# Kernel optimization log

Measured on AMD Instinct MI355X. Metric: run time of the kernel, lower is better.

Reference implementation:

```python
import jax, jax.numpy as jnp
import numpy as np

LENGTH, D, CHI, CLASSES = 784, 2, 128, 10
BATCH = 1024


def setup_inputs() -> dict:
    key = jax.random.key(0)
    k1, k2, k3 = jax.random.split(key, 3)
    # feature-mapped samples (batch, d, length), values in [0,1] like cossin map
    x = jax.random.uniform(k1, (BATCH, D, LENGTH), dtype=jnp.float32)
    # per-site residual weights; small init so the residual recurrence stays stable
    W = jax.random.normal(k2, (LENGTH, D, CHI, CHI), dtype=jnp.float32) * (0.01 / np.sqrt(CHI))
    # classifier matrix applied to the final hidden vector
    V = jax.random.normal(k3, (CHI, CLASSES), dtype=jnp.float32) / np.sqrt(CHI)
    return {"x": x, "W": W, "V": V}


def reference(x, W, V):
    # x: (B, d, L), W: (L, d, chi, chi), V: (chi, classes)
    B = x.shape[0]
    chi = W.shape[2]
    h0 = jnp.ones((B, chi), dtype=x.dtype)  # initial hidden bond vector

    xs = jnp.moveaxis(x, 2, 0)  # (L, B, d) so scan iterates over sites

    def site_step(h, inputs):
        xn, Wn = inputs  # xn: (B, d), Wn: (d, chi, chi)
        # residual MPS update: h <- h + sum_{s,a} x[n,s] W_n[s,a,b] h[a]
        h = h + jnp.einsum('ns,sab,na->nb', xn, Wn, h)
        return h, None

    h, _ = jax.lax.scan(site_step, h0, (xs, W))
    logits = h @ V  # (B, classes)
    return logits
```

## Files before the change

### kernel.cpp

```cpp
#include <hip/hip_runtime.h>

#define LL 784
#define CHI 128
#define CLS 10
#define BC 16
#define NBLK 64

typedef __attribute__((ext_vector_type(8))) short short8;
typedef __attribute__((ext_vector_type(4))) float floatx4;

__device__ inline unsigned int f2bf(float v) {
    unsigned int u = __float_as_uint(v);
    u += 0x7fffu + ((u >> 16) & 1u);
    return u >> 16;
}

__device__ inline void lds_barrier() {
    asm volatile("s_waitcnt lgkmcnt(0)\n\ts_barrier" ::: "memory");
}

__device__ inline float dpp_xor1(float v) {
    int r = __builtin_amdgcn_update_dpp(0, __float_as_int(v), 0xB1, 0xF, 0xF, true);
    return __int_as_float(r);
}

__global__ __launch_bounds__(256) void prep_kernel(const float* __restrict__ W,
                                                   uint4* __restrict__ ws4) {
    __shared__ float tile[32 * 132];
    const int b = blockIdx.x;
    const int n = b >> 3, s = (b >> 2) & 1, kt = b & 3;
    const float* Wp = W + ((size_t)(n * 2 + s) * CHI + kt * 32) * CHI;
    const int t = threadIdx.x;
    #pragma unroll
    for (int k = 0; k < 4; k++) {
        int v = t + k * 256;
        int a = v >> 5, c4 = v & 31;
        float4 val = *(const float4*)(Wp + a * CHI + c4 * 4);
        *(float4*)&tile[a * 132 + c4 * 4] = val;
    }
    __syncthreads();
    const int l = t & 63, f0 = t >> 6;
    const int m_ = l & 15, q_ = l >> 4;
    #pragma unroll
    for (int ff = 0; ff < 2; ff++) {
        int nt = f0 + ff * 4;
        const float* tp = &tile[(q_ * 8) * 132 + nt * 16 + m_];
        uint4 pk;
        pk.x = f2bf(tp[0 * 132]) | (f2bf(tp[1 * 132]) << 16);
        pk.y = f2bf(tp[2 * 132]) | (f2bf(tp[3 * 132]) << 16);
        pk.z = f2bf(tp[4 * 132]) | (f2bf(tp[5 * 132]) << 16);
        pk.w = f2bf(tp[6 * 132]) | (f2bf(tp[7 * 132]) << 16);
        ws4[(size_t)(((n * 8 + nt) * 2 + s) * 4 + kt) * 64 + l] = pk;
    }
}

__global__ __launch_bounds__(512) void mps_kernel(const float* __restrict__ x,
                                                  const unsigned short* __restrict__ ws,
                                                  const float* __restrict__ V,
                                                  float* __restrict__ out) {
    __shared__ short8 afbuf[2][256];
    __shared__ float xs[2][8][32];
    __shared__ float hfin[16 * 132];

    const int t = threadIdx.x;
    const int w = t >> 6, l = t & 63;
    const int m = l & 15, q = l >> 4;
    const int rb = blockIdx.x * BC;

    for (int i = t; i < 1024; i += 512)
        ((unsigned int*)&afbuf[0][0])[i] = 0x3F803F80u;

    const float* xrowp = x + (size_t)(rb + m) * (2 * LL) + (size_t)(q & 1) * LL;
    float4 xc2a, xc2b;
    if (l < 32) {
        float4 a0 = *(const float4*)(xrowp + 0);
        float4 b0 = *(const float4*)(xrowp + 4);
        float4 a1 = *(const float4*)(xrowp + 8);
        float4 b1 = *(const float4*)(xrowp + 12);
        float v0[8] = {a0.x, a0.y, a0.z, a0.w, b0.x, b0.y, b0.z, b0.w};
        float v1[8] = {a1.x, a1.y, a1.z, a1.w, b1.x, b1.y, b1.z, b1.w};
        #pragma unroll
        for (int k = 0; k < 8; k++) xs[0][k][(q & 1) * 16 + m] = v0[k];
        #pragma unroll
        for (int k = 0; k < 8; k++) xs[1][k][(q & 1) * 16 + m] = v1[k];
        xc2a = *(const float4*)(xrowp + 16);
        xc2b = *(const float4*)(xrowp + 20);
    }

    const unsigned short* wsw = ws + (size_t)w * 4096 + (size_t)l * 8;
    short8 bA[8], bB[8];
    #pragma unroll
    for (int f = 0; f < 8; f++) {
        bA[f] = *(const short8*)(wsw + (size_t)0 * 32768 + f * 512);
        bB[f] = *(const short8*)(wsw + (size_t)1 * 32768 + f * 512);
    }

    floatx4 hacc = (floatx4){1.f, 1.f, 1.f, 1.f};
    const int kt_w = w >> 1;
    const int qp_w = (w & 1) * 2 + (m >> 3);
    const int col2 = (m & 7) >> 1;

    __syncthreads();

#define SITE_BODY(NN, BUF) do {                                                   \
    const int n_ = (NN);                                                          \
    lds_barrier();                                                                \
    if ((n_ & 7) == 0 && n_ >= 8 && n_ + 8 < LL && l < 32) {                      \
        int par_ = ((n_ >> 3) + 1) & 1;                                           \
        float xv_[8] = {xc2a.x, xc2a.y, xc2a.z, xc2a.w,                           \
                        xc2b.x, xc2b.y, xc2b.z, xc2b.w};                          \
        _Pragma("unroll")                                                         \
        for (int k = 0; k < 8; k++) xs[par_][k][(q & 1) * 16 + m] = xv_[k];       \
        if (n_ + 16 < LL) {                                                       \
            xc2a = *(const float4*)(xrowp + n_ + 16);                             \
            xc2b = *(const float4*)(xrowp + n_ + 20);                             \
        }                                                                         \
    }                                                                             \
    short8 af0 = afbuf[n_ & 1][0 * 64 + l];                                       \
    short8 af1 = afbuf[n_ & 1][1 * 64 + l];                                       \
    short8 af2 = afbuf[n_ & 1][2 * 64 + l];                                       \
    short8 af3 = afbuf[n_ & 1][3 * 64 + l];                                       \
    floatx4 x0v = *(const floatx4*)&xs[(n_ >> 3) & 1][n_ & 7][q * 4];             \
    floatx4 x1v = *(const floatx4*)&xs[(n_ >> 3) & 1][n_ & 7][16 + q * 4];        \
    floatx4 z = (floatx4){0.f, 0.f, 0.f, 0.f};                                    \
    floatx4 a00 = __builtin_amdgcn_mfma_f32_16x16x32_bf16(af0, BUF[0], z, 0, 0, 0); \
    floatx4 a01 = __builtin_amdgcn_mfma_f32_16x16x32_bf16(af2, BUF[2], z, 0, 0, 0); \
    floatx4 a10 = __builtin_amdgcn_mfma_f32_16x16x32_bf16(af0, BUF[4], z, 0, 0, 0); \
    floatx4 a11 = __builtin_amdgcn_mfma_f32_16x16x32_bf16(af2, BUF[6], z, 0, 0, 0); \
    a00 = __builtin_amdgcn_mfma_f32_16x16x32_bf16(af1, BUF[1], a00, 0, 0, 0);     \
    a01 = __builtin_amdgcn_mfma_f32_16x16x32_bf16(af3, BUF[3], a01, 0, 0, 0);     \
    a10 = __builtin_amdgcn_mfma_f32_16x16x32_bf16(af1, BUF[5], a10, 0, 0, 0);     \
    a11 = __builtin_amdgcn_mfma_f32_16x16x32_bf16(af3, BUF[7], a11, 0, 0, 0);     \
    if (n_ + 2 < LL) {                                                            \
        _Pragma("unroll")                                                         \
        for (int f = 0; f < 8; f++)                                               \
            BUF[f] = *(const short8*)(wsw + (size_t)(n_ + 2) * 32768 + f * 512);  \
    }                                                                             \
    _Pragma("unroll")                                                             \
    for (int i = 0; i < 4; i++)                                                   \
        hacc[i] += x0v[i] * (a00[i] + a01[i]) + x1v[i] * (a10[i] + a11[i]);       \
    float pt0 = dpp_xor1(hacc[0]), pt1 = dpp_xor1(hacc[1]);                       \
    float pt2 = dpp_xor1(hacc[2]), pt3 = dpp_xor1(hacc[3]);                       \
    if (!(m & 1)) {                                                               \
        unsigned int* dst = (unsigned int*)&afbuf[(n_ + 1) & 1][0];               \
        int base_ = (kt_w * 64 + qp_w * 16 + q * 4) * 4 + col2;                   \
        dst[base_ + 0 * 4] = f2bf(hacc[0]) | (f2bf(pt0) << 16);                   \
        dst[base_ + 1 * 4] = f2bf(hacc[1]) | (f2bf(pt1) << 16);                   \
        dst[base_ + 2 * 4] = f2bf(hacc[2]) | (f2bf(pt2) << 16);                   \
        dst[base_ + 3 * 4] = f2bf(hacc[3]) | (f2bf(pt3) << 16);                   \
    }                                                                             \
} while (0)

    for (int n = 0; n < LL; n += 2) {
        SITE_BODY(n, bA);
        SITE_BODY(n + 1, bB);
    }
#undef SITE_BODY

    __syncthreads();

    #pragma unroll
    for (int i = 0; i < 4; i++)
        hfin[(q * 4 + i) * 132 + w * 16 + m] = hacc[i];
    __syncthreads();

    if (t < BC * CLS) {
        int r = t / CLS, cls = t % CLS;
        float sum = 0.f;
        for (int a = 0; a < CHI; a++) sum += hfin[r * 132 + a] * V[a * CLS + cls];
        out[(size_t)(rb + r) * CLS + cls] = sum;
    }
}

extern "C" void kernel_launch(void* const* d_in, const int* in_sizes, int n_in,
                              void* d_out, int out_size, void* d_ws, size_t ws_size,
                              hipStream_t stream) {
    const float* x = (const float*)d_in[0];
    const float* W = (const float*)d_in[1];
    const float* V = (const float*)d_in[2];
    float* out = (float*)d_out;

    prep_kernel<<<LL * 8, 256, 0, stream>>>(W, (uint4*)d_ws);
    mps_kernel<<<NBLK, 512, 0, stream>>>(x, (const unsigned short*)d_ws, V, out);
}
```

Measured before the change: 682.1 us.

## Transpose MFMA operands, halve waves per block, keep x in registers

The MPS recurrence kernel now uses 4 waves per block instead of 8. Each wave computes 32 output columns with 16 MFMAs per site, and the weight fragment becomes the A operand while the hidden state becomes the B operand. This layout lets each lane write its own packed bf16 hidden values straight to LDS via v_cvt_pk_bf16, with no DPP exchange or half-lane predication. Input x values are double-buffered in registers instead of staged through LDS, and the barrier now spans fewer waves. The cost is doubled register use for weight prefetch (32 short8 buffers) and less latency hiding from fewer waves.

After: 686.4 us. About the same (+0.6%).

```diff
diff --git a/kernel.cpp b/kernel.cpp
--- a/kernel.cpp
+++ b/kernel.cpp
@@ -19,9 +19,10 @@
     asm volatile("s_waitcnt lgkmcnt(0)\n\ts_barrier" ::: "memory");
 }
 
-__device__ inline float dpp_xor1(float v) {
-    int r = __builtin_amdgcn_update_dpp(0, __float_as_int(v), 0xB1, 0xF, 0xF, true);
-    return __int_as_float(r);
+__device__ inline unsigned int cvt_pk_bf16(float lo, float hi) {
+    unsigned int r;
+    asm("v_cvt_pk_bf16_f32 %0, %1, %2" : "=v"(r) : "v"(lo), "v"(hi));
+    return r;
 }
 
 __global__ __launch_bounds__(256) void prep_kernel(const float* __restrict__ W,
@@ -54,120 +55,123 @@
     }
 }
 
-__global__ __launch_bounds__(512) void mps_kernel(const float* __restrict__ x,
-                                                  const unsigned short* __restrict__ ws,
-                                                  const float* __restrict__ V,
-                                                  float* __restrict__ out) {
-    __shared__ short8 afbuf[2][256];
-    __shared__ float xs[2][8][32];
-    __shared__ float hfin[16 * 132];
+__global__ __launch_bounds__(256, 1) void mps_kernel(const float* __restrict__ x,
+                                                     const unsigned short* __restrict__ ws,
+                                                     const float* __restrict__ V,
+                                                     float* __restrict__ out) {
+    __shared__ short8 bfbuf[2][4][64];
+    __shared__ float hfin[BC * 136];
 
     const int t = threadIdx.x;
     const int w = t >> 6, l = t & 63;
     const int m = l & 15, q = l >> 4;
     const int rb = blockIdx.x * BC;
 
-    for (int i = t; i < 1024; i += 512)
-        ((unsigned int*)&afbuf[0][0])[i] = 0x3F803F80u;
+    for (int i = t; i < 1024; i += 256)
+        ((unsigned int*)&bfbuf[0][0][0])[i] = 0x3F803F80u;
 
-    const float* xrowp = x + (size_t)(rb + m) * (2 * LL) + (size_t)(q & 1) * LL;
-    float4 xc2a, xc2b;
-    if (l < 32) {
-        float4 a0 = *(const float4*)(xrowp + 0);
-        float4 b0 = *(const float4*)(xrowp + 4);
-        float4 a1 = *(const float4*)(xrowp + 8);
-        float4 b1 = *(const float4*)(xrowp + 12);
-        float v0[8] = {a0.x, a0.y, a0.z, a0.w, b0.x, b0.y, b0.z, b0.w};
-        float v1[8] = {a1.x, a1.y, a1.z, a1.w, b1.x, b1.y, b1.z, b1.w};
-        #pragma unroll
-        for (int k = 0; k < 8; k++) xs[0][k][(q & 1) * 16 + m] = v0[k];
-        #pragma unroll
-        for (int k = 0; k < 8; k++) xs[1][k][(q & 1) * 16 + m] = v1[k];
-        xc2a = *(const float4*)(xrowp + 16);
-        xc2b = *(const float4*)(xrowp + 20);
+    const float* xp0 = x + (size_t)(rb + m) * (2 * LL);
+    const float* xp1 = xp0 + LL;
+    float4 xA0, xA1, xA2, xA3, xB0, xB1, xB2, xB3;
+    xA0 = *(const float4*)(xp0 + 0);  xA1 = *(const float4*)(xp0 + 4);
+    xA2 = *(const float4*)(xp1 + 0);  xA3 = *(const float4*)(xp1 + 4);
+
+    const unsigned short* wsw = ws + (size_t)w * 8192 + (size_t)l * 8;
+    short8 bWA[16], bWB[16];
+    #pragma unroll
+    for (int f = 0; f < 16; f++) {
+        bWA[f] = *(const short8*)(wsw + (size_t)0 * 32768 + f * 512);
+        bWB[f] = *(const short8*)(wsw + (size_t)1 * 32768 + f * 512);
     }
 
-    const unsigned short* wsw = ws + (size_t)w * 4096 + (size_t)l * 8;
-    short8 bA[8], bB[8];
-    #pragma unroll
-    for (int f = 0; f < 8; f++) {
-        bA[f] = *(const short8*)(wsw + (size_t)0 * 32768 + f * 512);
-        bB[f] = *(const short8*)(wsw + (size_t)1 * 32768 + f * 512);
-    }
+    floatx4 hacc0 = (floatx4){1.f, 1.f, 1.f, 1.f};
+    floatx4 hacc1 = (floatx4){1.f, 1.f, 1.f, 1.f};
 
-    floatx4 hacc = (floatx4){1.f, 1.f, 1.f, 1.f};
-    const int kt_w = w >> 1;
-    const int qp_w = (w & 1) * 2 + (m >> 3);
-    const int col2 = (m & 7) >> 1;
+    unsigned int* const bfw = (unsigned int*)&bfbuf[0][0][0];
+    const int wr_dw = w * 256 + (q >> 1) * 64 + m * 4 + (q & 1) * 2;
 
-    __syncthreads();
-
-#define SITE_BODY(NN, BUF) do {                                                   \
-    const int n_ = (NN);                                                          \
-    lds_barrier();                                                                \
-    if ((n_ & 7) == 0 && n_ >= 8 && n_ + 8 < LL && l < 32) {                      \
-        int par_ = ((n_ >> 3) + 1) & 1;                                           \
-        float xv_[8] = {xc2a.x, xc2a.y, xc2a.z, xc2a.w,                           \
-                        xc2b.x, xc2b.y, xc2b.z, xc2b.w};                          \
-        _Pragma("unroll")                                                         \
-        for (int k = 0; k < 8; k++) xs[par_][k][(q & 1) * 16 + m] = xv_[k];       \
-        if (n_ + 16 < LL) {                                                       \
-            xc2a = *(const float4*)(xrowp + n_ + 16);                             \
-            xc2b = *(const float4*)(xrowp + n_ + 20);                             \
-        }                                                                         \
-    }                                                                             \
-    short8 af0 = afbuf[n_ & 1][0 * 64 + l];                                       \
-    short8 af1 = afbuf[n_ & 1][1 * 64 + l];                                       \
-    short8 af2 = afbuf[n_ & 1][2 * 64 + l];                                       \
-    short8 af3 = afbuf[n_ & 1][3 * 64 + l];                                       \
-    floatx4 x0v = *(const floatx4*)&xs[(n_ >> 3) & 1][n_ & 7][q * 4];             \
-    floatx4 x1v = *(const floatx4*)&xs[(n_ >> 3) & 1][n_ & 7][16 + q * 4];        \
-    floatx4 z = (floatx4){0.f, 0.f, 0.f, 0.f};                                    \
-    floatx4 a00 = __builtin_amdgcn_mfma_f32_16x16x32_bf16(af0, BUF[0], z, 0, 0, 0); \
-    floatx4 a01 = __builtin_amdgcn_mfma_f32_16x16x32_bf16(af2, BUF[2], z, 0, 0, 0); \
-    floatx4 a10 = __builtin_amdgcn_mfma_f32_16x16x32_bf16(af0, BUF[4], z, 0, 0, 0); \
-    floatx4 a11 = __builtin_amdgcn_mfma_f32_16x16x32_bf16(af2, BUF[6], z, 0, 0, 0); \
-    a00 = __builtin_amdgcn_mfma_f32_16x16x32_bf16(af1, BUF[1], a00, 0, 0, 0);     \
-    a01 = __builtin_amdgcn_mfma_f32_16x16x32_bf16(af3, BUF[3], a01, 0, 0, 0);     \
-    a10 = __builtin_amdgcn_mfma_f32_16x16x32_bf16(af1, BUF[5], a10, 0, 0, 0);     \
-    a11 = __builtin_amdgcn_mfma_f32_16x16x32_bf16(af3, BUF[7], a11, 0, 0, 0);     \
-    if (n_ + 2 < LL) {                                                            \
-        _Pragma("unroll")                                                         \
-        for (int f = 0; f < 8; f++)                                               \
-            BUF[f] = *(const short8*)(wsw + (size_t)(n_ + 2) * 32768 + f * 512);  \
-    }                                                                             \
-    _Pragma("unroll")                                                             \
-    for (int i = 0; i < 4; i++)                                                   \
-        hacc[i] += x0v[i] * (a00[i] + a01[i]) + x1v[i] * (a10[i] + a11[i]);       \
-    float pt0 = dpp_xor1(hacc[0]), pt1 = dpp_xor1(hacc[1]);                       \
-    float pt2 = dpp_xor1(hacc[2]), pt3 = dpp_xor1(hacc[3]);                       \
-    if (!(m & 1)) {                                                               \
-        unsigned int* dst = (unsigned int*)&afbuf[(n_ + 1) & 1][0];               \
-        int base_ = (kt_w * 64 + qp_w * 16 + q * 4) * 4 + col2;                   \
-        dst[base_ + 0 * 4] = f2bf(hacc[0]) | (f2bf(pt0) << 16);                   \
-        dst[base_ + 1 * 4] = f2bf(hacc[1]) | (f2bf(pt1) << 16);                   \
-        dst[base_ + 2 * 4] = f2bf(hacc[2]) | (f2bf(pt2) << 16);                   \
-        dst[base_ + 3 * 4] = f2bf(hacc[3]) | (f2bf(pt3) << 16);                   \
-    }                                                                             \
+#define SITE_BODY(NN, PAR, WBUF, X0, X1) do {                                       \
+    lds_barrier();                                                                  \
+    short8 bf0 = bfbuf[PAR][0][l];                                                  \
+    short8 bf1 = bfbuf[PAR][1][l];                                                  \
+    short8 bf2 = bfbuf[PAR][2][l];                                                  \
+    short8 bf3 = bfbuf[PAR][3][l];                                                  \
+    floatx4 z = (floatx4){0.f, 0.f, 0.f, 0.f};                                      \
+    floatx4 p0l = __builtin_amdgcn_mfma_f32_16x16x32_bf16(WBUF[0],  bf0, z, 0,0,0); \
+    floatx4 p0h = __builtin_amdgcn_mfma_f32_16x16x32_bf16(WBUF[2],  bf2, z, 0,0,0); \
+    floatx4 p1l = __builtin_amdgcn_mfma_f32_16x16x32_bf16(WBUF[4],  bf0, z, 0,0,0); \
+    floatx4 p1h = __builtin_amdgcn_mfma_f32_16x16x32_bf16(WBUF[6],  bf2, z, 0,0,0); \
+    floatx4 q0l = __builtin_amdgcn_mfma_f32_16x16x32_bf16(WBUF[8],  bf0, z, 0,0,0); \
+    floatx4 q0h = __builtin_amdgcn_mfma_f32_16x16x32_bf16(WBUF[10], bf2, z, 0,0,0); \
+    floatx4 q1l = __builtin_amdgcn_mfma_f32_16x16x32_bf16(WBUF[12], bf0, z, 0,0,0); \
+    floatx4 q1h = __builtin_amdgcn_mfma_f32_16x16x32_bf16(WBUF[14], bf2, z, 0,0,0); \
+    p0l = __builtin_amdgcn_mfma_f32_16x16x32_bf16(WBUF[1],  bf1, p0l, 0,0,0);       \
+    p0h = __builtin_amdgcn_mfma_f32_16x16x32_bf16(WBUF[3],  bf3, p0h, 0,0,0);       \
+    p1l = __builtin_amdgcn_mfma_f32_16x16x32_bf16(WBUF[5],  bf1, p1l, 0,0,0);       \
+    p1h = __builtin_amdgcn_mfma_f32_16x16x32_bf16(WBUF[7],  bf3, p1h, 0,0,0);       \
+    q0l = __builtin_amdgcn_mfma_f32_16x16x32_bf16(WBUF[9],  bf1, q0l, 0,0,0);       \
+    q0h = __builtin_amdgcn_mfma_f32_16x16x32_bf16(WBUF[11], bf3, q0h, 0,0,0);       \
+    q1l = __builtin_amdgcn_mfma_f32_16x16x32_bf16(WBUF[13], bf1, q1l, 0,0,0);       \
+    q1h = __builtin_amdgcn_mfma_f32_16x16x32_bf16(WBUF[15], bf3, q1h, 0,0,0);       \
+    if ((NN) + 2 < LL) {                                                            \
+        _Pragma("unroll")                                                           \
+        for (int f = 0; f < 16; f++)                                                \
+            WBUF[f] = *(const short8*)(wsw + (size_t)((NN) + 2) * 32768 + f * 512); \
+    }                                                                               \
+    _Pragma("unroll")                                                               \
+    for (int i = 0; i < 4; i++) {                                                   \
+        hacc0[i] += (X0) * (p0l[i] + p0h[i]) + (X1) * (p1l[i] + p1h[i]);            \
+        hacc1[i] += (X0) * (q0l[i] + q0h[i]) + (X1) * (q1l[i] + q1h[i]);            \
+    }                                                                               \
+    uint2 pk0, pk1;                                                                 \
+    pk0.x = cvt_pk_bf16(hacc0[0], hacc0[1]);                                        \
+    pk0.y = cvt_pk_bf16(hacc0[2], hacc0[3]);                                        \
+    pk1.x = cvt_pk_bf16(hacc1[0], hacc1[1]);                                        \
+    pk1.y = cvt_pk_bf16(hacc1[2], hacc1[3]);                                        \
+    *(uint2*)&bfw[((PAR) ^ 1) * 1024 + wr_dw]       = pk0;                          \
+    *(uint2*)&bfw[((PAR) ^ 1) * 1024 + 128 + wr_dw] = pk1;                          \
 } while (0)
 
-    for (int n = 0; n < LL; n += 2) {
-        SITE_BODY(n, bA);
-        SITE_BODY(n + 1, bB);
+    for (int nb = 0; nb < LL; nb += 16) {
+        if (nb + 8 < LL) {
+            xB0 = *(const float4*)(xp0 + nb + 8);
+            xB1 = *(const float4*)(xp0 + nb + 12);
+            xB2 = *(const float4*)(xp1 + nb + 8);
+            xB3 = *(const float4*)(xp1 + nb + 12);
+        }
+        SITE_BODY(nb + 0,  0, bWA, xA0.x, xA2.x);
+        SITE_BODY(nb + 1,  1, bWB, xA0.y, xA2.y);
+        SITE_BODY(nb + 2,  0, bWA, xA0.z, xA2.z);
+        SITE_BODY(nb + 3,  1, bWB, xA0.w, xA2.w);
+        SITE_BODY(nb + 4,  0, bWA, xA1.x, xA3.x);
+        SITE_BODY(nb + 5,  1, bWB, xA1.y, xA3.y);
+        SITE_BODY(nb + 6,  0, bWA, xA1.z, xA3.z);
+        SITE_BODY(nb + 7,  1, bWB, xA1.w, xA3.w);
+        if (nb + 16 < LL) {
+            xA0 = *(const float4*)(xp0 + nb + 16);
+            xA1 = *(const float4*)(xp0 + nb + 20);
+            xA2 = *(const float4*)(xp1 + nb + 16);
+            xA3 = *(const float4*)(xp1 + nb + 20);
+        }
+        SITE_BODY(nb + 8,  0, bWA, xB0.x, xB2.x);
+        SITE_BODY(nb + 9,  1, bWB, xB0.y, xB2.y);
+        SITE_BODY(nb + 10, 0, bWA, xB0.z, xB2.z);
+        SITE_BODY(nb + 11, 1, bWB, xB0.w, xB2.w);
+        SITE_BODY(nb + 12, 0, bWA, xB1.x, xB3.x);
+        SITE_BODY(nb + 13, 1, bWB, xB1.y, xB3.y);
+        SITE_BODY(nb + 14, 0, bWA, xB1.z, xB3.z);
+        SITE_BODY(nb + 15, 1, bWB, xB1.w, xB3.w);
     }
 #undef SITE_BODY
 
-    __syncthreads();
-
-    #pragma unroll
-    for (int i = 0; i < 4; i++)
-        hfin[(q * 4 + i) * 132 + w * 16 + m] = hacc[i];
+    *(floatx4*)&hfin[m * 136 + w * 32 + q * 4]      = hacc0;
+    *(floatx4*)&hfin[m * 136 + w * 32 + 16 + q * 4] = hacc1;
     __syncthreads();
 
     if (t < BC * CLS) {
         int r = t / CLS, cls = t % CLS;
         float sum = 0.f;
-        for (int a = 0; a < CHI; a++) sum += hfin[r * 132 + a] * V[a * CLS + cls];
+        for (int a = 0; a < CHI; a++) sum += hfin[r * 136 + a] * V[a * CLS + cls];
         out[(size_t)(rb + r) * CLS + cls] = sum;
     }
 }
@@ -181,5 +185,5 @@
     float* out = (float*)d_out;
 
     prep_kernel<<<LL * 8, 256, 0, stream>>>(W, (uint4*)d_ws);
-    mps_kernel<<<NBLK, 512, 0, stream>>>(x, (const unsigned short*)d_ws, V, out);
+    mps_kernel<<<NBLK, 256, 0, stream>>>(x, (const unsigned short*)d_ws, V, out);
 }
```
